# Kernel tuning notes

Hardware: AMD Instinct MI355X
Metric: run time of the kernel (lower is better)

The kernel has to match this reference:

```python
import jax, jax.numpy as jnp
import numpy as np

HD, CD, BN = 128, 192, 16       # hidden_dim, context_dim, bin_num
OC = 2 * HD                     # ProjectionInputDepth out_chs
GC = HD + OC + CD               # GRU conv in-channels = hidden + (out_chs + context)
MAX_TREE_DEPTH = 6


def conv2d(x, w, b, ph, pw):
    y = jax.lax.conv_general_dilated(
        x, w, window_strides=(1, 1), padding=((ph, ph), (pw, pw)),
        dimension_numbers=('NCHW', 'OIHW', 'NCHW'))
    return y + b[None, :, None, None]


def setup_inputs():
    key = jax.random.key(0)
    B, H, W = 2, 120, 160
    ki = iter(jax.random.split(key, 20))
    def w(shape, s=0.05):
        return jax.random.normal(next(ki), shape, jnp.float32) * s
    z = lambda c: jnp.zeros((c,), jnp.float32)
    return {
        'depth': jax.random.uniform(next(ki), (B, 1, H, W), jnp.float32) * 80.0,
        'context': jax.random.normal(next(ki), (B, CD, H, W), jnp.float32),
        'gru_hidden': jax.random.normal(next(ki), (B, HD, H, W), jnp.float32),
        'encd1_w': w((HD, BN, 7, 7)), 'encd1_b': z(HD),
        'encd2_w': w((HD, HD, 3, 3)), 'encd2_b': z(HD),
        'encd3_w': w((HD, HD, 3, 3)), 'encd3_b': z(HD),
        'encd4_w': w((OC, HD, 3, 3)), 'encd4_b': z(OC),
        'convz1_w': w((HD, GC, 1, 5)), 'convz1_b': z(HD),
        'convr1_w': w((HD, GC, 1, 5)), 'convr1_b': z(HD),
        'convq1_w': w((HD, GC, 1, 5)), 'convq1_b': z(HD),
        'convz2_w': w((HD, GC, 5, 1)), 'convz2_b': z(HD),
        'convr2_w': w((HD, GC, 5, 1)), 'convr2_b': z(HD),
        'convq2_w': w((HD, GC, 5, 1)), 'convq2_b': z(HD),
        'ph1_w': w((HD, HD, 3, 3)), 'ph1_b': z(HD),
        'ph2_w': w((BN, HD, 3, 3)), 'ph2_b': z(BN),
        'bin_num': 16, 'min_depth': 0, 'max_depth': 80,
    }


def reference(depth, context, gru_hidden,
              encd1_w, encd1_b, encd2_w, encd2_b, encd3_w, encd3_b, encd4_w, encd4_b,
              convz1_w, convz1_b, convr1_w, convr1_b, convq1_w, convq1_b,
              convz2_w, convz2_b, convr2_w, convr2_b, convq2_w, convq2_b,
              ph1_w, ph1_b, ph2_w, ph2_b,
              bin_num, min_depth, max_depth):
    sg = jax.lax.stop_gradient
    B, _, H, W = depth.shape
    n = int(bin_num)
    mn, mx = float(min_depth), float(max_depth)
    # get_iebins: uniform bin edges via cumsum of constant intervals, (B, n+1, H, W)
    iv0 = jnp.concatenate([jnp.full((B, 1, H, W), mn, jnp.float32),
                           jnp.full((B, n, H, W), (mx - mn) / n, jnp.float32)], axis=1)
    bin_edges = jnp.cumsum(iv0, axis=1)
    current_depths = 0.5 * (bin_edges[:, :-1] + bin_edges[:, 1:])
    h = gru_hidden
    rs, cs, us = [], [], []
    for _ in range(MAX_TREE_DEPTH):
        cd = sg(current_depths)
        # ProjectionInputDepth
        d = jax.nn.relu(conv2d(cd, encd1_w, encd1_b, 3, 3))
        d = jax.nn.relu(conv2d(d, encd2_w, encd2_b, 1, 1))
        d = jax.nn.relu(conv2d(d, encd3_w, encd3_b, 1, 1))
        d = jax.nn.relu(conv2d(d, encd4_w, encd4_b, 1, 1))
        x = jnp.concatenate([d, context], axis=1)
        # SepConvGRU: horizontal (1,5) pass then vertical (5,1) pass
        hx = jnp.concatenate([h, x], axis=1)
        zg = jax.nn.sigmoid(conv2d(hx, convz1_w, convz1_b, 0, 2))
        rg = jax.nn.sigmoid(conv2d(hx, convr1_w, convr1_b, 0, 2))
        q = jnp.tanh(conv2d(jnp.concatenate([rg * h, x], axis=1), convq1_w, convq1_b, 0, 2))
        h = (1.0 - zg) * h + zg * q
        hx = jnp.concatenate([h, x], axis=1)
        zg = jax.nn.sigmoid(conv2d(hx, convz2_w, convz2_b, 2, 0))
        rg = jax.nn.sigmoid(conv2d(hx, convr2_w, convr2_b, 2, 0))
        q = jnp.tanh(conv2d(jnp.concatenate([rg * h, x], axis=1), convq2_w, convq2_b, 2, 0))
        h = (1.0 - zg) * h + zg * q
        # PHead -> per-bin probabilities
        prob = jax.nn.softmax(conv2d(jax.nn.relu(conv2d(h, ph1_w, ph1_b, 1, 1)), ph2_w, ph2_b, 1, 1), axis=1)
        depth_r = jnp.sum(prob * cd, axis=1, keepdims=True)        # (B,1,H,W)
        rs.append(depth_r)
        unc = jnp.sqrt(jnp.sum(prob * (cd - depth_r) ** 2, axis=1, keepdims=True))
        us.append(unc)
        # get_label: bin i with edges[i] <= d < edges[i+1]; 0 if out of range
        dv = sg(depth_r[:, 0])                                     # (B,H,W)
        cnt = jnp.sum((dv[:, None] >= bin_edges[:, 1:n]).astype(jnp.int32), axis=1)
        label = jnp.where(dv >= bin_edges[:, n], 0, cnt)[:, None]  # (B,1,H,W)
        cs.append(jnp.take_along_axis(cd, label, axis=1))
        # update_bins (mode 'direct', no grad): recenter on depth_r, width = uncertainty
        dr, um = sg(depth_r), sg(unc)
        start = jnp.maximum(dr - 0.5 * um, mn)
        ivals = jnp.concatenate([start, jnp.broadcast_to(um / n, (B, n, H, W))], axis=1)
        bin_edges = jnp.clip(jnp.cumsum(ivals, axis=1), mn, mx)
        current_depths = 0.5 * (bin_edges[:, :-1] + bin_edges[:, 1:])
    # stacked lists: (3, 6, B, 1, H, W) = [pred_depths_r, pred_depths_c, uncertainty_maps]
    return jnp.stack([jnp.stack(rs), jnp.stack(cs), jnp.stack(us)])
```

## Files before the change

### kernel.cpp

```cpp
#include <hip/hip_runtime.h>
#include <hip/hip_bf16.h>


#define HD  128
#define CDC 192
#define BN  16
#define OCH 256
#define GC  576
#define NB  2
#define HH  120
#define WW  160
#define HW  (HH*WW)
#define BHW (NB*HW)
#define PXT (BHW/128)
#define GXP (((PXT+7)/8)*8)
#define TPX (GXP/8)
#define PWW 168
#define PHH 126
#define PHW (PWW*PHH)
#define POFF(y,x) (((y)+3)*PWW + (x) + 4)

__device__ __forceinline__ float2 ldf2(const float* p){ return *(const float2*)p; }
__device__ __forceinline__ void stf2(float* p, float a, float b){
  *(float2*)p = make_float2(a,b);
}

typedef float f2 __attribute__((ext_vector_type(2), aligned(4)));
typedef float f4 __attribute__((ext_vector_type(4), aligned(16)));
__device__ __forceinline__ f2 ldpo(const float* __restrict__ base, const unsigned off){
  return *(const f2*)(base + off);
}
template<int NP>
__device__ __forceinline__ void ldwn(const float* __restrict__ p, f2* w){
  #pragma unroll
  for (int k=0;k<NP;k+=2){
    const f4 v = *(const f4*)(p + 2*k);
    w[k]   = f2{v.x, v.y};
    w[k+1] = f2{v.z, v.w};
  }
}

__device__ __forceinline__ void pkfma2(f2& a, const f2 v, const f2 w){
  a = __builtin_elementwise_fma(v, w, a);
}

__global__ __launch_bounds__(256) void k_zero32(float* __restrict__ p, const size_t n){
  const size_t i = (size_t)blockIdx.x*256 + threadIdx.x;
  for (size_t k=i; k<n; k += (size_t)gridDim.x*256) p[k] = 0.f;
}
__global__ __launch_bounds__(256) void k_zero64(double* __restrict__ p, const size_t n){
  const size_t i = (size_t)blockIdx.x*256 + threadIdx.x;
  for (size_t k=i; k<n; k += (size_t)gridDim.x*256) p[k] = 0.0;
}

__global__ __launch_bounds__(256) void k_pad(const float* __restrict__ src,
        float* __restrict__ dst, const int nplanes){
  const int i = blockIdx.x*256 + threadIdx.x;
  if (i >= nplanes*HW) return;
  const int bc = i / HW, r = i - bc*HW;
  const int y = r / WW, x = r - y*WW;
  dst[(size_t)bc*PHW + POFF(y,x)] = src[i];
}

__global__ __launch_bounds__(256) void k_init(const float* __restrict__ gh,
        float* __restrict__ h, double* __restrict__ edges, double* __restrict__ cdp){
  const int i = blockIdx.x*256 + threadIdx.x;
  const int nh = NB*HD*HW;
  if (i < nh){
    const int bc = i / HW, r = i - bc*HW;
    const int y = r / WW, x = r - y*WW;
    h[(size_t)bc*PHW + POFF(y,x)] = gh[i];
  }
  if (i < BHW){
    const int b = i / HW, r = i - b*HW;
    const int y = r / WW, x = r - y*WW;
    const int pr = POFF(y,x);
    double e = 0.0;
    #pragma unroll
    for (int k=0;k<BN;++k){
      edges[(b*(BN+1)+k)*HW + r] = e;
      cdp[((size_t)b*BN+k)*PHW + pr] = e + 2.5;
      e += 5.0;
    }
    edges[(b*(BN+1)+BN)*HW + r] = e;
  }
}

__global__ __launch_bounds__(256) void k_wxpose(const float* __restrict__ w,
        float* __restrict__ wt, const int Cout, const int CIN, const int TAPS,
        const int n){
  const int i = blockIdx.x*256 + threadIdx.x;
  if (i >= n) return;
  const int ct = CIN*TAPS;
  const int o = i / ct;
  const int rem = i - o*ct;
  const int c = rem / TAPS;
  const int t = rem - c*TAPS;
  wt[((size_t)c*TAPS + t)*Cout + o] = w[i];
}

template<int GY>
__device__ __forceinline__ bool blk_decode(int& xs, int& yg){
  const int id  = blockIdx.x;
  const int xcd = id & 7;
  const int s   = id >> 3;
  yg = s & (GY-1);
  const int k = s / GY;
  xs = xcd*TPX + k;
  return xs < PXT;
}

__device__ __forceinline__ void pair_decode(const int xs, int& b, int& r0, int& po){
  const int lane = threadIdx.x & 63;
  const int pb = xs*128;
  b = pb / HW;
  r0 = pb - b*HW + 2*lane;
  const int y = r0 / WW, x = r0 - y*WW;
  po = POFF(y,x);
}

__global__ __launch_bounds__(256) void k_e1(const double* __restrict__ cdp,
        const float* __restrict__ wt, const float* __restrict__ bias,
        float* __restrict__ out){
  const int NACC = 8, NP = NACC/2;
  int xs, yg;
  if (!blk_decode<4>(xs, yg)) return;
  const int wvu = __builtin_amdgcn_readfirstlane((int)(threadIdx.x >> 6));
  const int ow0 = (yg*4 + wvu)*NACC;
  int b, r0, po;
  pair_decode(xs, b, r0, po);
  double acc[2][NACC];
  #pragma unroll
  for (int j=0;j<NACC;++j){
    const double bj = (double)bias[ow0+j];
    acc[0][j]=bj; acc[1][j]=bj;
  }
  const double* inb = cdp + (size_t)b*16*PHW;
  #pragma unroll 1
  for (int t=0;t<49;++t){
    const unsigned pot = (unsigned)(po + (t/7 - 3)*PWW + (t%7 - 3));
    f2 ca[2][NP];
    #pragma unroll
    for (int p=0;p<NP;++p){ ca[0][p]=f2{0.f,0.f}; ca[1][p]=f2{0.f,0.f}; }
    const float* wr = wt + (size_t)t*HD + ow0;
    #pragma unroll 4
    for (int c=0;c<16;++c){
      const double* pp = inb + (size_t)c*PHW;
      const float v0 = (float)pp[pot];
      const float v1 = (float)pp[pot+1u];
      const f2 v00 = {v0, v0};
      const f2 v11 = {v1, v1};
      f2 wp_[NP];
      ldwn<NP>(wr, wp_);
      #pragma unroll
      for (int p=0;p<NP;++p){
        pkfma2(ca[0][p], v00, wp_[p]);
        pkfma2(ca[1][p], v11, wp_[p]);
      }
      wr += (size_t)49*HD;
    }
    #pragma unroll
    for (int p=0;p<NP;++p){
      acc[0][2*p]  +=(double)ca[0][p].x; acc[0][2*p+1]+=(double)ca[0][p].y;
      acc[1][2*p]  +=(double)ca[1][p].x; acc[1][2*p+1]+=(double)ca[1][p].y;
    }
  }
  #pragma unroll
  for (int j=0;j<NACC;++j){
    double v0 = acc[0][j]; v0 = v0>0.0?v0:0.0;
    double v1 = acc[1][j]; v1 = v1>0.0?v1:0.0;
    stf2(out + ((size_t)b*HD + ow0 + j)*PHW + po, (float)v0, (float)v1);
  }
}

template<int NACC,int GY,int ACT>
__global__ __launch_bounds__(256) void k_fc3(const float* __restrict__ in,
        const float* __restrict__ wt, const float* __restrict__ bias,
        float* __restrict__ out, const int Cout){
  const int NP = NACC/2;
  int xs, yg;
  if (!blk_decode<GY>(xs, yg)) return;
  const int wvu = __builtin_amdgcn_readfirstlane((int)(threadIdx.x >> 6));
  const int ow0 = (yg*4 + wvu)*NACC;
  int b, r0, po;
  pair_decode(xs, b, r0, po);
  double acc[2][NACC];
  #pragma unroll
  for (int j=0;j<NACC;++j){
    const double bj = (double)bias[ow0+j];
    acc[0][j]=bj; acc[1][j]=bj;
  }
  const float* inb = in + (size_t)b*128*PHW;
  #pragma unroll 1
  for (int t=0;t<9;++t){
    const unsigned pot = (unsigned)(po + (t/3 - 1)*PWW + (t%3 - 1));
    #pragma unroll 1
    for (int c0=0;c0<128;c0+=32){
      f2 ca[2][NP];
      #pragma unroll
      for (int p=0;p<NP;++p){ ca[0][p]=f2{0.f,0.f}; ca[1][p]=f2{0.f,0.f}; }
      const float* wr = wt + ((size_t)c0*9 + t)*Cout + ow0;
      #pragma unroll 8
      for (int c=0;c<32;++c){
        const f2 v = ldpo(inb + (size_t)(c0+c)*PHW, pot);
        const f2 v00 = {v.x, v.x};
        const f2 v11 = {v.y, v.y};
        f2 wp_[NP];
        ldwn<NP>(wr, wp_);
        #pragma unroll
        for (int p=0;p<NP;++p){
          pkfma2(ca[0][p], v00, wp_[p]);
          pkfma2(ca[1][p], v11, wp_[p]);
        }
        wr += (size_t)9*Cout;
      }
      #pragma unroll
      for (int p=0;p<NP;++p){
        acc[0][2*p]  +=(double)ca[0][p].x; acc[0][2*p+1]+=(double)ca[0][p].y;
        acc[1][2*p]  +=(double)ca[1][p].x; acc[1][2*p+1]+=(double)ca[1][p].y;
      }
    }
  }
  #pragma unroll
  for (int j=0;j<NACC;++j){
    double v0 = acc[0][j], v1 = acc[1][j];
    if (ACT==1){ v0 = v0>0.0?v0:0.0; v1 = v1>0.0?v1:0.0; }
    stf2(out + ((size_t)b*Cout + ow0 + j)*PHW + po, (float)v0, (float)v1);
  }
}

template<int C,int NACC>
__device__ __forceinline__ void seg2(const float* __restrict__ plane, const unsigned pot,
    const float* __restrict__ wz0, const float* __restrict__ wr0,
    double az[2][NACC], double ar[2][NACC]){
  const int NP = NACC/2;
  #pragma unroll 1
  for (int c0=0;c0<C;c0+=32){
    f2 cz[2][NP], cr[2][NP];
    #pragma unroll
    for (int p=0;p<NP;++p){
      cz[0][p]=f2{0.f,0.f}; cz[1][p]=f2{0.f,0.f};
      cr[0][p]=f2{0.f,0.f}; cr[1][p]=f2{0.f,0.f};
    }
    const float* wz = wz0 + (size_t)c0*5*HD;
    const float* wr = wr0 + (size_t)c0*5*HD;
    #pragma unroll 4
    for (int c=0;c<32;++c){
      const f2 v = ldpo(plane + (size_t)(c0+c)*PHW, pot);
      const f2 v00 = {v.x, v.x};
      const f2 v11 = {v.y, v.y};
      f2 wzp[NP], wrp[NP];
      ldwn<NP>(wz, wzp);
      ldwn<NP>(wr, wrp);
      #pragma unroll
      for (int p=0;p<NP;++p){
        pkfma2(cz[0][p], v00, wzp[p]); pkfma2(cz[1][p], v11, wzp[p]);
        pkfma2(cr[0][p], v00, wrp[p]); pkfma2(cr[1][p], v11, wrp[p]);
      }
      wz += 5*HD; wr += 5*HD;
    }
    #pragma unroll
    for (int p=0;p<NP;++p){
      az[0][2*p]+=(double)cz[0][p].x; az[0][2*p+1]+=(double)cz[0][p].y;
      az[1][2*p]+=(double)cz[1][p].x; az[1][2*p+1]+=(double)cz[1][p].y;
      ar[0][2*p]+=(double)cr[0][p].x; ar[0][2*p+1]+=(double)cr[0][p].y;
      ar[1][2*p]+=(double)cr[1][p].x; ar[1][2*p+1]+=(double)cr[1][p].y;
    }
  }
}
template<int C,int NACC>
__device__ __forceinline__ void seg3(const float* __restrict__ plane, const unsigned pot,
    const float* __restrict__ wz0, const float* __restrict__ wr0,
    const float* __restrict__ wq0,
    double az[2][NACC], double ar[2][NACC], double aq[2][NACC]){
  const int NP = NACC/2;
  #pragma unroll 1
  for (int c0=0;c0<C;c0+=32){
    f2 cz[2][NP], cr[2][NP], cq[2][NP];
    #pragma unroll
    for (int p=0;p<NP;++p){
      cz[0][p]=f2{0.f,0.f}; cz[1][p]=f2{0.f,0.f};
      cr[0][p]=f2{0.f,0.f}; cr[1][p]=f2{0.f,0.f};
      cq[0][p]=f2{0.f,0.f}; cq[1][p]=f2{0.f,0.f};
    }
    const float* wz = wz0 + (size_t)c0*5*HD;
    const float* wr = wr0 + (size_t)c0*5*HD;
    const float* wq = wq0 + (size_t)c0*5*HD;
    #pragma unroll 4
    for (int c=0;c<32;++c){
      const f2 v = ldpo(plane + (size_t)(c0+c)*PHW, pot);
      const f2 v00 = {v.x, v.x};
      const f2 v11 = {v.y, v.y};
      f2 wzp[NP], wrp[NP], wqp[NP];
      ldwn<NP>(wz, wzp);
      ldwn<NP>(wr, wrp);
      ldwn<NP>(wq, wqp);
      #pragma unroll
      for (int p=0;p<NP;++p){
        pkfma2(cz[0][p], v00, wzp[p]); pkfma2(cz[1][p], v11, wzp[p]);
        pkfma2(cr[0][p], v00, wrp[p]); pkfma2(cr[1][p], v11, wrp[p]);
        pkfma2(cq[0][p], v00, wqp[p]); pkfma2(cq[1][p], v11, wqp[p]);
      }
      wz += 5*HD; wr += 5*HD; wq += 5*HD;
    }
    #pragma unroll
    for (int p=0;p<NP;++p){
      az[0][2*p]+=(double)cz[0][p].x; az[0][2*p+1]+=(double)cz[0][p].y;
      az[1][2*p]+=(double)cz[1][p].x; az[1][2*p+1]+=(double)cz[1][p].y;
      ar[0][2*p]+=(double)cr[0][p].x; ar[0][2*p+1]+=(double)cr[0][p].y;
      ar[1][2*p]+=(double)cr[1][p].x; ar[1][2*p+1]+=(double)cr[1][p].y;
      aq[0][2*p]+=(double)cq[0][p].x; aq[0][2*p+1]+=(double)cq[0][p].y;
      aq[1][2*p]+=(double)cq[1][p].x; aq[1][2*p+1]+=(double)cq[1][p].y;
    }
  }
}
template<int C,int NACC>
__device__ __forceinline__ void seg1(const float* __restrict__ plane, const unsigned pot,
    const float* __restrict__ wq0, double aq[2][NACC]){
  const int NP = NACC/2;
  #pragma unroll 1
  for (int c0=0;c0<C;c0+=32){
    f2 cq[2][NP];
    #pragma unroll
    for (int p=0;p<NP;++p){ cq[0][p]=f2{0.f,0.f}; cq[1][p]=f2{0.f,0.f}; }
    const float* wq = wq0 + (size_t)c0*5*HD;
    #pragma unroll 8
    for (int c=0;c<32;++c){
      const f2 v = ldpo(plane + (size_t)(c0+c)*PHW, pot);
      const f2 v00 = {v.x, v.x};
      const f2 v11 = {v.y, v.y};
      f2 wqp[NP];
      ldwn<NP>(wq, wqp);
      #pragma unroll
      for (int p=0;p<NP;++p){
        pkfma2(cq[0][p], v00, wqp[p]);
        pkfma2(cq[1][p], v11, wqp[p]);
      }
      wq += 5*HD;
    }
    #pragma unroll
    for (int p=0;p<NP;++p){
      aq[0][2*p]+=(double)cq[0][p].x; aq[0][2*p+1]+=(double)cq[0][p].y;
      aq[1][2*p]+=(double)cq[1][p].x; aq[1][2*p+1]+=(double)cq[1][p].y;
    }
  }
}

template<int VERT>
__global__ __launch_bounds__(256) void k_zrx(
    const float* __restrict__ h, const float* __restrict__ d4,
    const float* __restrict__ ctxp,
    const float* __restrict__ wtz, const float* __restrict__ wtr,
    const float* __restrict__ wtq,
    const float* __restrict__ bz, const float* __restrict__ br,
    const float* __restrict__ bq,
    float* __restrict__ zg, float* __restrict__ rgh, float* __restrict__ qx){
  const int NACC = 4;
  int xs, yg;
  if (!blk_decode<8>(xs, yg)) return;
  const int wvu = __builtin_amdgcn_readfirstlane((int)(threadIdx.x >> 6));
  const int ow0 = (yg*4 + wvu)*NACC;
  int b, r0, po;
  pair_decode(xs, b, r0, po);
  double az[2][NACC], ar[2][NACC], aq[2][NACC];
  #pragma unroll
  for (int j=0;j<NACC;++j){
    const double bzj=(double)bz[ow0+j], brj=(double)br[ow0+j], bqj=(double)bq[ow0+j];
    az[0][j]=bzj; az[1][j]=bzj; ar[0][j]=brj; ar[1][j]=brj; aq[0][j]=bqj; aq[1][j]=bqj;
  }
  const float* hb = h   + (size_t)b*HD *PHW;
  const float* db = d4  + (size_t)b*OCH*PHW;
  const float* cb = ctxp+ (size_t)b*CDC*PHW;
  #pragma unroll 1
  for (int t=0;t<5;++t){
    const unsigned pot = (unsigned)(po + (VERT ? (t-2)*PWW : (t-2)));
    seg2<HD ,NACC>(hb, pot, wtz + (size_t)t*HD + ow0,
                            wtr + (size_t)t*HD + ow0, az, ar);
    seg3<OCH,NACC>(db, pot, wtz + ((size_t)HD*5 + t)*HD + ow0,
                            wtr + ((size_t)HD*5 + t)*HD + ow0,
                            wtq + ((size_t)HD*5 + t)*HD + ow0, az, ar, aq);
    seg3<CDC,NACC>(cb, pot, wtz + ((size_t)(HD+OCH)*5 + t)*HD + ow0,
                            wtr + ((size_t)(HD+OCH)*5 + t)*HD + ow0,
                            wtq + ((size_t)(HD+OCH)*5 + t)*HD + ow0, az, ar, aq);
  }
  #pragma unroll
  for (int j=0;j<NACC;++j){
    const size_t pp = ((size_t)b*HD + ow0 + j)*PHW + po;
    const float2 hv = ldf2(h + pp);
    const double z0 = 1.0/(1.0+exp(-az[0][j])), z1 = 1.0/(1.0+exp(-az[1][j]));
    const double g0 = (1.0/(1.0+exp(-ar[0][j]))) * (double)hv.x;
    const double g1 = (1.0/(1.0+exp(-ar[1][j]))) * (double)hv.y;
    stf2(zg  + pp, (float)z0, (float)z1);
    stf2(rgh + pp, (float)g0, (float)g1);
    stf2(qx + ((size_t)b*HD + ow0 + j)*HW + r0, (float)aq[0][j], (float)aq[1][j]);
  }
}

template<int VERT>
__global__ __launch_bounds__(256) void k_qh(
    const float* __restrict__ rgh, const float* __restrict__ wtq,
    const float* __restrict__ qx, const float* __restrict__ zg,
    float* __restrict__ h){
  const int NACC = 8;
  int xs, yg;
  if (!blk_decode<4>(xs, yg)) return;
  const int wvu = __builtin_amdgcn_readfirstlane((int)(threadIdx.x >> 6));
  const int ow0 = (yg*4 + wvu)*NACC;
  int b, r0, po;
  pair_decode(xs, b, r0, po);
  double aq[2][NACC];
  #pragma unroll
  for (int j=0;j<NACC;++j){
    const float2 q0 = ldf2(qx + ((size_t)b*HD + ow0 + j)*HW + r0);
    aq[0][j] = (double)q0.x; aq[1][j] = (double)q0.y;
  }
  const float* gb = rgh + (size_t)b*HD*PHW;
  #pragma unroll 1
  for (int t=0;t<5;++t){
    const unsigned pot = (unsigned)(po + (VERT ? (t-2)*PWW : (t-2)));
    seg1<HD,NACC>(gb, pot, wtq + (size_t)t*HD + ow0, aq);
  }
  #pragma unroll
  for (int j=0;j<NACC;++j){
    const size_t pp = ((size_t)b*HD + ow0 + j)*PHW + po;
    const float2 zv = ldf2(zg + pp);
    const float2 hv = ldf2(h  + pp);
    const double z0=(double)zv.x, z1=(double)zv.y;
    const double n0 = (1.0-z0)*(double)hv.x + z0*tanh(aq[0][j]);
    const double n1 = (1.0-z1)*(double)hv.y + z1*tanh(aq[1][j]);
    stf2(h + pp, (float)n0, (float)n1);
  }
}

__global__ __launch_bounds__(256) void k_stats(const float* __restrict__ lg,
    double* __restrict__ edges, double* __restrict__ cdp, float* __restrict__ out,
    const int it){
  const int px = blockIdx.x*256 + threadIdx.x;
  const int b = px / HW, r = px - b*HW;
  const int y = r / WW, x = r - y*WW;
  const int pr = POFF(y,x);
  double l[BN], p[BN], c[BN];
  double m = -1e300;
  #pragma unroll
  for (int k=0;k<BN;++k){ l[k] = (double)lg[((size_t)b*BN+k)*PHW + pr]; m = l[k]>m?l[k]:m; }
  double s = 0.0;
  #pragma unroll
  for (int k=0;k<BN;++k){ p[k] = exp(l[k]-m); s += p[k]; }
  double dr = 0.0;
  #pragma unroll
  for (int k=0;k<BN;++k){ c[k] = cdp[((size_t)b*BN+k)*PHW + pr]; p[k] = p[k]/s; dr += p[k]*c[k]; }
  double var = 0.0;
  #pragma unroll
  for (int k=0;k<BN;++k){ const double d = c[k]-dr; var += p[k]*(d*d); }
  const double un = sqrt(var);
  int cnt = 0;
  #pragma unroll
  for (int k=1;k<BN;++k) cnt += (dr >= edges[(b*(BN+1)+k)*HW + r]) ? 1 : 0;
  const double etop = edges[(b*(BN+1)+BN)*HW + r];
  const int label = (dr >= etop) ? 0 : cnt;
  double csv = c[0];
  #pragma unroll
  for (int k=1;k<BN;++k) csv = (label==k) ? c[k] : csv;
  out[((0*6+it)*NB + b)*HW + r] = (float)dr;
  out[((1*6+it)*NB + b)*HW + r] = (float)csv;
  out[((2*6+it)*NB + b)*HW + r] = (float)un;
  const double start = dr - 0.5*un > 0.0 ? dr - 0.5*un : 0.0;
  const double step = un * (1.0/BN);
  double e = start;
  double prev = e < 0.0 ? 0.0 : (e > 80.0 ? 80.0 : e);
  edges[(b*(BN+1)+0)*HW + r] = prev;
  #pragma unroll
  for (int k=1;k<=BN;++k){
    e = e + step;
    const double ec = e < 0.0 ? 0.0 : (e > 80.0 ? 80.0 : e);
    edges[(b*(BN+1)+k)*HW + r] = ec;
    cdp[((size_t)b*BN + (k-1))*PHW + pr] = 0.5*(prev + ec);
    prev = ec;
  }
}

extern "C" void kernel_launch(void* const* d_in, const int* in_sizes, int n_in,
                              void* d_out, int out_size, void* d_ws, size_t ws_size,
                              hipStream_t stream){
  const float* ctx = (const float*)d_in[1];
  const float* gh  = (const float*)d_in[2];
  const float *e1w=(const float*)d_in[3],  *e1b=(const float*)d_in[4];
  const float *e2w=(const float*)d_in[5],  *e2b=(const float*)d_in[6];
  const float *e3w=(const float*)d_in[7],  *e3b=(const float*)d_in[8];
  const float *e4w=(const float*)d_in[9],  *e4b=(const float*)d_in[10];
  const float *z1w=(const float*)d_in[11], *z1b=(const float*)d_in[12];
  const float *r1w=(const float*)d_in[13], *r1b=(const float*)d_in[14];
  const float *q1w=(const float*)d_in[15], *q1b=(const float*)d_in[16];
  const float *z2w=(const float*)d_in[17], *z2b=(const float*)d_in[18];
  const float *r2w=(const float*)d_in[19], *r2b=(const float*)d_in[20];
  const float *q2w=(const float*)d_in[21], *q2b=(const float*)d_in[22];
  const float *p1w=(const float*)d_in[23], *p1b=(const float*)d_in[24];
  const float *p2w=(const float*)d_in[25], *p2b=(const float*)d_in[26];
  float* out = (float*)d_out;

  double* edges = (double*)d_ws;
  double* cdp   = edges + (size_t)NB*(BN+1)*HW;
  float* fb    = (float*)(cdp + (size_t)NB*BN*PHW);
  float* hp    = fb;
  float* d4p   = hp    + (size_t)NB*HD *PHW;
  float* bufAp = d4p   + (size_t)NB*OCH*PHW;
  float* bufBp = bufAp + (size_t)NB*HD *PHW;
  float* ctxp  = bufBp + (size_t)NB*HD *PHW;
  float* lgtsp = ctxp  + (size_t)NB*CDC*PHW;
  const size_t npad32 = (size_t)NB*(HD+OCH+HD+HD+CDC+BN)*PHW;
  float* qx   = lgtsp + (size_t)NB*BN*PHW;
  float* wp   = qx + (size_t)NB*HD*HW;
  float* we1 = wp;              wp += (size_t)HD*16*49;
  float* we2 = wp;              wp += (size_t)HD*HD*9;
  float* we3 = wp;              wp += (size_t)HD*HD*9;
  float* we4 = wp;              wp += (size_t)OCH*HD*9;
  float* wz1 = wp;              wp += (size_t)HD*GC*5;
  float* wr1 = wp;              wp += (size_t)HD*GC*5;
  float* wq1 = wp;              wp += (size_t)HD*GC*5;
  float* wz2 = wp;              wp += (size_t)HD*GC*5;
  float* wr2 = wp;              wp += (size_t)HD*GC*5;
  float* wq2 = wp;              wp += (size_t)HD*GC*5;
  float* wp1 = wp;              wp += (size_t)HD*HD*9;
  float* wp2 = wp;              wp += (size_t)16*HD*9;

  const dim3 blk(256);

  k_zero32<<<dim3(2048), blk, 0, stream>>>(fb, npad32);
  k_zero64<<<dim3(1024), blk, 0, stream>>>(cdp, (size_t)NB*BN*PHW);

  #define XP(src,dst,Cout_,CIN_,TAPS_) { const int n=(Cout_)*(CIN_)*(TAPS_); \
    k_wxpose<<<dim3((n+255)/256), blk, 0, stream>>>(src, dst, Cout_, CIN_, TAPS_, n); }
  XP(e1w, we1, HD, 16, 49); XP(e2w, we2, HD, HD, 9); XP(e3w, we3, HD, HD, 9);
  XP(e4w, we4, OCH, HD, 9);
  XP(z1w, wz1, HD, GC, 5); XP(r1w, wr1, HD, GC, 5); XP(q1w, wq1, HD, GC, 5);
  XP(z2w, wz2, HD, GC, 5); XP(r2w, wr2, HD, GC, 5); XP(q2w, wq2, HD, GC, 5);
  XP(p1w, wp1, HD, HD, 9); XP(p2w, wp2, 16, HD, 9);
  #undef XP

  k_pad<<<dim3((NB*CDC*HW+255)/256), blk, 0, stream>>>(ctx, ctxp, NB*CDC);
  k_init<<<dim3((NB*HD*HW+255)/256), blk, 0, stream>>>(gh, hp, edges, cdp);

  const int G8 = GXP*8, G4 = GXP*4, G1 = GXP;
  const int PXB = BHW/256;

  for (int it=0; it<6; ++it){
    k_e1        <<<dim3(G4), blk, 0, stream>>>(cdp,   we1, e1b, bufAp);
    k_fc3<8,4,1><<<dim3(G4), blk, 0, stream>>>(bufAp, we2, e2b, bufBp, HD);
    k_fc3<8,4,1><<<dim3(G4), blk, 0, stream>>>(bufBp, we3, e3b, bufAp, HD);
    k_fc3<8,8,1><<<dim3(G8), blk, 0, stream>>>(bufAp, we4, e4b, d4p,  OCH);
    k_zrx<0><<<dim3(G8), blk, 0, stream>>>(hp, d4p, ctxp, wz1, wr1, wq1,
                                           z1b, r1b, q1b, bufAp, bufBp, qx);
    k_qh <0><<<dim3(G4), blk, 0, stream>>>(bufBp, wq1, qx, bufAp, hp);
    k_zrx<1><<<dim3(G8), blk, 0, stream>>>(hp, d4p, ctxp, wz2, wr2, wq2,
                                           z2b, r2b, q2b, bufAp, bufBp, qx);
    k_qh <1><<<dim3(G4), blk, 0, stream>>>(bufBp, wq2, qx, bufAp, hp);
    k_fc3<8,4,1><<<dim3(G4), blk, 0, stream>>>(hp,    wp1, p1b, bufAp, HD);
    k_fc3<4,1,0><<<dim3(G1), blk, 0, stream>>>(bufAp, wp2, p2b, lgtsp, 16);
    k_stats<<<dim3(PXB), blk, 0, stream>>>(lgtsp, edges, cdp, out, it);
  }
}
```

Baseline: 25.17 ms.

## Split fused z/r/q-input GRU conv kernel into separate z/r and q-input kernels

Splits the fused GRU gate kernel into two kernels. k_zr computes the z and r gates with 8 output channels per wave at half the grid, and k_qx computes the q input-projection separately, also with 8 channels per wave. This raises per-thread reuse of each loaded input pixel across output channels and adds an occupancy hint of 5 on k_zr. The cost is an extra launch and re-reading the d4 and context planes in a second kernel.

```diff
diff --git a/kernel.cpp b/kernel.cpp
--- a/kernel.cpp
+++ b/kernel.cpp
@@ -269,52 +269,6 @@
   }
 }
 template<int C,int NACC>
-__device__ __forceinline__ void seg3(const float* __restrict__ plane, const unsigned pot,
-    const float* __restrict__ wz0, const float* __restrict__ wr0,
-    const float* __restrict__ wq0,
-    double az[2][NACC], double ar[2][NACC], double aq[2][NACC]){
-  const int NP = NACC/2;
-  #pragma unroll 1
-  for (int c0=0;c0<C;c0+=32){
-    f2 cz[2][NP], cr[2][NP], cq[2][NP];
-    #pragma unroll
-    for (int p=0;p<NP;++p){
-      cz[0][p]=f2{0.f,0.f}; cz[1][p]=f2{0.f,0.f};
-      cr[0][p]=f2{0.f,0.f}; cr[1][p]=f2{0.f,0.f};
-      cq[0][p]=f2{0.f,0.f}; cq[1][p]=f2{0.f,0.f};
-    }
-    const float* wz = wz0 + (size_t)c0*5*HD;
-    const float* wr = wr0 + (size_t)c0*5*HD;
-    const float* wq = wq0 + (size_t)c0*5*HD;
-    #pragma unroll 4
-    for (int c=0;c<32;++c){
-      const f2 v = ldpo(plane + (size_t)(c0+c)*PHW, pot);
-      const f2 v00 = {v.x, v.x};
-      const f2 v11 = {v.y, v.y};
-      f2 wzp[NP], wrp[NP], wqp[NP];
-      ldwn<NP>(wz, wzp);
-      ldwn<NP>(wr, wrp);
-      ldwn<NP>(wq, wqp);
-      #pragma unroll
-      for (int p=0;p<NP;++p){
-        pkfma2(cz[0][p], v00, wzp[p]); pkfma2(cz[1][p], v11, wzp[p]);
-        pkfma2(cr[0][p], v00, wrp[p]); pkfma2(cr[1][p], v11, wrp[p]);
-        pkfma2(cq[0][p], v00, wqp[p]); pkfma2(cq[1][p], v11, wqp[p]);
-      }
-      wz += 5*HD; wr += 5*HD; wq += 5*HD;
-    }
-    #pragma unroll
-    for (int p=0;p<NP;++p){
-      az[0][2*p]+=(double)cz[0][p].x; az[0][2*p+1]+=(double)cz[0][p].y;
-      az[1][2*p]+=(double)cz[1][p].x; az[1][2*p+1]+=(double)cz[1][p].y;
-      ar[0][2*p]+=(double)cr[0][p].x; ar[0][2*p+1]+=(double)cr[0][p].y;
-      ar[1][2*p]+=(double)cr[1][p].x; ar[1][2*p+1]+=(double)cr[1][p].y;
-      aq[0][2*p]+=(double)cq[0][p].x; aq[0][2*p+1]+=(double)cq[0][p].y;
-      aq[1][2*p]+=(double)cq[1][p].x; aq[1][2*p+1]+=(double)cq[1][p].y;
-    }
-  }
-}
-template<int C,int NACC>
 __device__ __forceinline__ void seg1(const float* __restrict__ plane, const unsigned pot,
     const float* __restrict__ wq0, double aq[2][NACC]){
   const int NP = NACC/2;
@@ -347,26 +301,25 @@
 }
 
 template<int VERT>
-__global__ __launch_bounds__(256) void k_zrx(
+__global__ __launch_bounds__(256,5) void k_zr(
     const float* __restrict__ h, const float* __restrict__ d4,
     const float* __restrict__ ctxp,
     const float* __restrict__ wtz, const float* __restrict__ wtr,
-    const float* __restrict__ wtq,
     const float* __restrict__ bz, const float* __restrict__ br,
-    const float* __restrict__ bq,
-    float* __restrict__ zg, float* __restrict__ rgh, float* __restrict__ qx){
-  const int NACC = 4;
+    float* __restrict__ zg, float* __restrict__ rgh){
+  const int NACC = 8;
   int xs, yg;
-  if (!blk_decode<8>(xs, yg)) return;
+  if (!blk_decode<4>(xs, yg)) return;
   const int wvu = __builtin_amdgcn_readfirstlane((int)(threadIdx.x >> 6));
   const int ow0 = (yg*4 + wvu)*NACC;
   int b, r0, po;
   pair_decode(xs, b, r0, po);
-  double az[2][NACC], ar[2][NACC], aq[2][NACC];
-  #pragma unroll
-  for (int j=0;j<NACC;++j){
-    const double bzj=(double)bz[ow0+j], brj=(double)br[ow0+j], bqj=(double)bq[ow0+j];
-    az[0][j]=bzj; az[1][j]=bzj; ar[0][j]=brj; ar[1][j]=brj; aq[0][j]=bqj; aq[1][j]=bqj;
+  (void)r0;
+  double az[2][NACC], ar[2][NACC];
+  #pragma unroll
+  for (int j=0;j<NACC;++j){
+    const double bzj=(double)bz[ow0+j], brj=(double)br[ow0+j];
+    az[0][j]=bzj; az[1][j]=bzj; ar[0][j]=brj; ar[1][j]=brj;
   }
   const float* hb = h   + (size_t)b*HD *PHW;
   const float* db = d4  + (size_t)b*OCH*PHW;
@@ -376,12 +329,10 @@
     const unsigned pot = (unsigned)(po + (VERT ? (t-2)*PWW : (t-2)));
     seg2<HD ,NACC>(hb, pot, wtz + (size_t)t*HD + ow0,
                             wtr + (size_t)t*HD + ow0, az, ar);
-    seg3<OCH,NACC>(db, pot, wtz + ((size_t)HD*5 + t)*HD + ow0,
-                            wtr + ((size_t)HD*5 + t)*HD + ow0,
-                            wtq + ((size_t)HD*5 + t)*HD + ow0, az, ar, aq);
-    seg3<CDC,NACC>(cb, pot, wtz + ((size_t)(HD+OCH)*5 + t)*HD + ow0,
-                            wtr + ((size_t)(HD+OCH)*5 + t)*HD + ow0,
-                            wtq + ((size_t)(HD+OCH)*5 + t)*HD + ow0, az, ar, aq);
+    seg2<OCH,NACC>(db, pot, wtz + ((size_t)HD*5 + t)*HD + ow0,
+                            wtr + ((size_t)HD*5 + t)*HD + ow0, az, ar);
+    seg2<CDC,NACC>(cb, pot, wtz + ((size_t)(HD+OCH)*5 + t)*HD + ow0,
+                            wtr + ((size_t)(HD+OCH)*5 + t)*HD + ow0, az, ar);
   }
   #pragma unroll
   for (int j=0;j<NACC;++j){
@@ -392,6 +343,37 @@
     const double g1 = (1.0/(1.0+exp(-ar[1][j]))) * (double)hv.y;
     stf2(zg  + pp, (float)z0, (float)z1);
     stf2(rgh + pp, (float)g0, (float)g1);
+  }
+}
+
+template<int VERT>
+__global__ __launch_bounds__(256) void k_qx(
+    const float* __restrict__ d4, const float* __restrict__ ctxp,
+    const float* __restrict__ wtq, const float* __restrict__ bq,
+    float* __restrict__ qx){
+  const int NACC = 8;
+  int xs, yg;
+  if (!blk_decode<4>(xs, yg)) return;
+  const int wvu = __builtin_amdgcn_readfirstlane((int)(threadIdx.x >> 6));
+  const int ow0 = (yg*4 + wvu)*NACC;
+  int b, r0, po;
+  pair_decode(xs, b, r0, po);
+  double aq[2][NACC];
+  #pragma unroll
+  for (int j=0;j<NACC;++j){
+    const double bqj=(double)bq[ow0+j];
+    aq[0][j]=bqj; aq[1][j]=bqj;
+  }
+  const float* db = d4  + (size_t)b*OCH*PHW;
+  const float* cb = ctxp+ (size_t)b*CDC*PHW;
+  #pragma unroll 1
+  for (int t=0;t<5;++t){
+    const unsigned pot = (unsigned)(po + (VERT ? (t-2)*PWW : (t-2)));
+    seg1<OCH,NACC>(db, pot, wtq + ((size_t)HD*5 + t)*HD + ow0, aq);
+    seg1<CDC,NACC>(cb, pot, wtq + ((size_t)(HD+OCH)*5 + t)*HD + ow0, aq);
+  }
+  #pragma unroll
+  for (int j=0;j<NACC;++j){
     stf2(qx + ((size_t)b*HD + ow0 + j)*HW + r0, (float)aq[0][j], (float)aq[1][j]);
   }
 }
@@ -548,11 +530,13 @@
     k_fc3<8,4,1><<<dim3(G4), blk, 0, stream>>>(bufAp, we2, e2b, bufBp, HD);
     k_fc3<8,4,1><<<dim3(G4), blk, 0, stream>>>(bufBp, we3, e3b, bufAp, HD);
     k_fc3<8,8,1><<<dim3(G8), blk, 0, stream>>>(bufAp, we4, e4b, d4p,  OCH);
-    k_zrx<0><<<dim3(G8), blk, 0, stream>>>(hp, d4p, ctxp, wz1, wr1, wq1,
-                                           z1b, r1b, q1b, bufAp, bufBp, qx);
+    k_zr <0><<<dim3(G4), blk, 0, stream>>>(hp, d4p, ctxp, wz1, wr1,
+                                           z1b, r1b, bufAp, bufBp);
+    k_qx <0><<<dim3(G4), blk, 0, stream>>>(d4p, ctxp, wq1, q1b, qx);
     k_qh <0><<<dim3(G4), blk, 0, stream>>>(bufBp, wq1, qx, bufAp, hp);
-    k_zrx<1><<<dim3(G8), blk, 0, stream>>>(hp, d4p, ctxp, wz2, wr2, wq2,
-                                           z2b, r2b, q2b, bufAp, bufBp, qx);
+    k_zr <1><<<dim3(G4), blk, 0, stream>>>(hp, d4p, ctxp, wz2, wr2,
+                                           z2b, r2b, bufAp, bufBp);
+    k_qx <1><<<dim3(G4), blk, 0, stream>>>(d4p, ctxp, wq2, q2b, qx);
     k_qh <1><<<dim3(G4), blk, 0, stream>>>(bufBp, wq2, qx, bufAp, hp);
     k_fc3<8,4,1><<<dim3(G4), blk, 0, stream>>>(hp,    wp1, p1b, bufAp, HD);
     k_fc3<4,1,0><<<dim3(G1), blk, 0, stream>>>(bufAp, wp2, p2b, lgtsp, 16);
```

Measured after the change: 33.88 ms. +34.6%, slower.
